# Optimization experiments

Measured on AMD Instinct MI355X. Metric: run time of the kernel, lower is better.

## Reference

```python
import jax, jax.numpy as jnp
import numpy as np

N_NODES = 100000
N_EDGES = 3200000
N_FEAT = 256
N_FILT = 256


def setup_inputs() -> dict:
    key = jax.random.key(0)
    k1, k2, k3, k4, k5 = jax.random.split(key, 5)
    # Xavier-normal-ish filters: std = sqrt(2/(fan_in+fan_out))
    std = (2.0 / (N_FEAT + N_FILT)) ** 0.5
    filters = jax.random.normal(k1, (N_FEAT, N_FILT), dtype=jnp.float32) * std
    x = jax.random.normal(k2, (N_NODES, N_FEAT), dtype=jnp.float32)
    edge_row = jax.random.randint(k3, (N_EDGES,), 0, N_NODES, dtype=jnp.int32)
    edge_col = jax.random.randint(k4, (N_EDGES,), 0, N_NODES, dtype=jnp.int32)
    edge_weight = jax.random.uniform(k5, (N_EDGES,), dtype=jnp.float32)
    return {"x": x, "filters": filters, "edge_row": edge_row,
            "edge_col": edge_col, "edge_weight": edge_weight}


def reference(x, filters, edge_row, edge_col, edge_weight):
    # XF = x @ filters  -> [N, K]
    XF = jnp.matmul(x, filters)
    # out = transform @ XF, transform given in COO form:
    # out[r] = sum_{e: row[e]==r} weight[e] * XF[col[e]]
    msgs = edge_weight[:, None] * XF[edge_col]          # [E, K] gather
    out = jax.ops.segment_sum(msgs, edge_row, num_segments=N_NODES)  # [N, K] scatter-add
    return out
```

## Files before the change

### kernel.cpp

```cpp
#include <hip/hip_runtime.h>

#define NF 256
#define NK 256
#define NBKT 512
#define TILEA 8192

typedef __attribute__((ext_vector_type(8))) short bf16x8;
typedef __attribute__((ext_vector_type(4))) float f32x4;

__device__ __forceinline__ ushort f2bf(float f) {
  uint u = __float_as_uint(f);
  return (ushort)((u + 0x7fffu + ((u >> 16) & 1u)) >> 16);
}
__device__ __forceinline__ float bf2f(ushort h) {
  return __uint_as_float(((uint)h) << 16);
}

__global__ __launch_bounds__(256) void prelude(const float* __restrict__ F,
                                               ushort* __restrict__ Ft,
                                               const int* __restrict__ erow,
                                               int* __restrict__ bcnt, int nE) {
  __shared__ int h[NBKT];
  if (blockIdx.x < NF) {
    int k = blockIdx.x;
    int n = threadIdx.x;
    Ft[(size_t)n * NF + k] = f2bf(F[(size_t)k * NK + n]);
    return;
  }
  const int bid = blockIdx.x - NF;
  const int nb = gridDim.x - NF;
  h[threadIdx.x] = 0;
  h[threadIdx.x + 256] = 0;
  __syncthreads();
  for (int e = bid * 256 + threadIdx.x; e < nE; e += nb * 256)
    atomicAdd(&h[erow[e] >> 8], 1);
  __syncthreads();
  int v0 = h[threadIdx.x], v1 = h[threadIdx.x + 256];
  if (v0) atomicAdd(&bcnt[threadIdx.x], v0);
  if (v1) atomicAdd(&bcnt[threadIdx.x + 256], v1);
}

__global__ __launch_bounds__(256) void gemm_mfma(const float* __restrict__ x,
                                                 const ushort* __restrict__ Ft,
                                                 ushort* __restrict__ XFh, int M) {
  __shared__ ushort As[32 * NF];
  const int t = threadIdx.x;
  const int row0 = blockIdx.x * 32;

  const float4* xv = (const float4*)(x + (size_t)row0 * NF);
#pragma unroll
  for (int j = 0; j < 8; ++j) {
    int idx = j * 256 + t;
    int r = idx >> 6;
    int c4 = idx & 63;
    float4 v = make_float4(0.f, 0.f, 0.f, 0.f);
    if (row0 + r < M) v = xv[idx];
    ushort4 hh = make_ushort4(f2bf(v.x), f2bf(v.y), f2bf(v.z), f2bf(v.w));
    uint boff = (uint)(r * 512 + c4 * 8);
    boff ^= (uint)((r & 7) << 4);
    *(ushort4*)((char*)As + boff) = hh;
  }
  __syncthreads();

  const int lane = t & 63;
  const int wv = t >> 6;
  const int arow = lane & 15;
  const int kg = lane >> 4;

  bf16x8 afr[2][8];
#pragma unroll
  for (int rt = 0; rt < 2; ++rt) {
#pragma unroll
    for (int kk = 0; kk < 8; ++kk) {
      int r = rt * 16 + arow;
      uint boff = (uint)(r * 512 + kk * 64 + kg * 16);
      boff ^= (uint)((r & 7) << 4);
      afr[rt][kk] = *(const bf16x8*)((const char*)As + boff);
    }
  }

  f32x4 acc[2][4];
#pragma unroll
  for (int rt = 0; rt < 2; ++rt)
#pragma unroll
    for (int f = 0; f < 4; ++f) acc[rt][f] = (f32x4){0.f, 0.f, 0.f, 0.f};

  const int ncol0 = wv * 64;
#pragma unroll
  for (int f = 0; f < 4; ++f) {
    const ushort* bp = Ft + (size_t)(ncol0 + f * 16 + arow) * NF + kg * 8;
#pragma unroll
    for (int kk = 0; kk < 8; ++kk) {
      bf16x8 bfr = *(const bf16x8*)(bp + kk * 32);
      acc[0][f] = __builtin_amdgcn_mfma_f32_16x16x32_bf16(afr[0][kk], bfr, acc[0][f], 0, 0, 0);
      acc[1][f] = __builtin_amdgcn_mfma_f32_16x16x32_bf16(afr[1][kk], bfr, acc[1][f], 0, 0, 0);
    }
  }

#pragma unroll
  for (int rt = 0; rt < 2; ++rt) {
#pragma unroll
    for (int f = 0; f < 4; ++f) {
      int col = ncol0 + f * 16 + arow;
#pragma unroll
      for (int rg = 0; rg < 4; ++rg) {
        int row = row0 + rt * 16 + kg * 4 + rg;
        if (row < M) XFh[(size_t)row * NK + col] = f2bf(acc[rt][f][rg]);
      }
    }
  }
}

__global__ __launch_bounds__(512) void scan_bbase(const int* __restrict__ bcnt,
                                                  int* __restrict__ bbase,
                                                  int* __restrict__ bcursor) {
  __shared__ int s[NBKT];
  int t = threadIdx.x;
  int v = bcnt[t];
  s[t] = v;
  __syncthreads();
  for (int d = 1; d < NBKT; d <<= 1) {
    int tmp = (t >= d) ? s[t - d] : 0;
    __syncthreads();
    s[t] += tmp;
    __syncthreads();
  }
  int excl = s[t] - v;
  bbase[t] = excl;
  bcursor[t * 16] = excl;
}

__global__ __launch_bounds__(512) void bin_coarse(const int* __restrict__ erow,
                                                  const int* __restrict__ ecol,
                                                  const float* __restrict__ ew,
                                                  int* __restrict__ bcursor,
                                                  int2* __restrict__ tmpCW, int nE) {
  __shared__ int h[NBKT];
  __shared__ int lb[NBKT];
  __shared__ int gb[NBKT];
  __shared__ int2 pay[TILEA];
  const int t = threadIdx.x;
  const int base = blockIdx.x * TILEA;

  h[t] = 0;
  __syncthreads();

  int rnk[16], bb[16], loc[16];
#pragma unroll
  for (int k = 0; k < 16; ++k) {
    int i = base + k * 512 + t;
    rnk[k] = -1; bb[k] = 0; loc[k] = 0;
    if (i < nE) {
      int row = erow[i];
      bb[k] = row >> 8;
      loc[k] = row & 255;
      rnk[k] = atomicAdd(&h[bb[k]], 1);
    }
  }
  __syncthreads();

  int hv = h[t];
  lb[t] = hv;
  __syncthreads();
  for (int d = 1; d < NBKT; d <<= 1) {
    int tmp = (t >= d) ? lb[t - d] : 0;
    __syncthreads();
    lb[t] += tmp;
    __syncthreads();
  }
  int ex = lb[t] - hv;
  __syncthreads();
  lb[t] = ex;
  if (hv > 0) gb[t] = atomicAdd(&bcursor[t * 16], hv);
  __syncthreads();

#pragma unroll
  for (int k = 0; k < 16; ++k) {
    int i = base + k * 512 + t;
    if (i < nE) {
      int pos = lb[bb[k]] + rnk[k];
      pay[pos] = make_int2(ecol[i] | (loc[k] << 20), __float_as_int(ew[i]));
    }
  }
  __syncthreads();

  const int wv = t >> 6, lane = t & 63;
  for (int b = wv; b < NBKT; b += 8) {
    int len = h[b];
    if (!len) continue;
    int lbase = lb[b], gbase = gb[b];
    for (int off = lane; off < len; off += 64)
      tmpCW[gbase + off] = pay[lbase + off];
  }
}

__global__ __launch_bounds__(256) void bin_fine(const int2* __restrict__ tmpCW,
                                                const int* __restrict__ bbase,
                                                const int* __restrict__ bcnt,
                                                int* __restrict__ offsets,
                                                int2* __restrict__ cw,
                                                int nNodes, int nE) {
  __shared__ int hist[256];
  __shared__ int cur[256];
  const int b = blockIdx.x;
  const int t = threadIdx.x;
  const int base = bbase[b];
  const int n = bcnt[b];

  hist[t] = 0;
  __syncthreads();
  for (int i = t; i < n; i += 256)
    atomicAdd(&hist[((uint)tmpCW[base + i].x) >> 20], 1);
  __syncthreads();

  int hv = hist[t];
  cur[t] = hv;
  __syncthreads();
  for (int d = 1; d < 256; d <<= 1) {
    int tmp = (t >= d) ? cur[t - d] : 0;
    __syncthreads();
    cur[t] += tmp;
    __syncthreads();
  }
  int ex = cur[t] - hv;
  __syncthreads();
  cur[t] = ex;
  int node = (b << 8) + t;
  if (node < nNodes) offsets[node] = base + ex;
  if (b == 0 && t == 0) offsets[nNodes] = nE;
  __syncthreads();

  for (int i = t; i < n; i += 256) {
    int2 v = tmpCW[base + i];
    int local = ((uint)v.x) >> 20;
    int d = base + atomicAdd(&cur[local], 1);
    cw[d] = make_int2(v.x & 0xFFFFF, v.y);
  }
}

__global__ __launch_bounds__(256) void gather_bf16(const ushort* __restrict__ XFh,
                                                   const int* __restrict__ offsets,
                                                   const int2* __restrict__ cw,
                                                   f32x4* __restrict__ outv,
                                                   int nNodes) {
  const int lane = threadIdx.x & 63;
  const int node = (blockIdx.x * blockDim.x + threadIdx.x) >> 6;
  if (node >= nNodes) return;
  const int start = offsets[node];
  const int end = offsets[node + 1];
  const ushort4* XV = (const ushort4*)XFh;

  float ax = 0.f, ay = 0.f, az = 0.f, aw = 0.f;
  for (int base = start; base < end; base += 64) {
    int n = end - base;
    if (n > 64) n = 64;
    int2 e = make_int2(0, 0);
    if (lane < n) {
      long long raw = __builtin_nontemporal_load((const long long*)(cw + base + lane));
      e.x = (int)(raw & 0xFFFFFFFFll);
      e.y = (int)(raw >> 32);
    }
    int skey = (lane < n) ? ((e.x << 6) | lane) : ((0xFFFFF << 6) | lane);
    int sval = e.y;
#pragma unroll
    for (int k = 2; k <= 64; k <<= 1) {
#pragma unroll
      for (int j = k >> 1; j > 0; j >>= 1) {
        int pk = __shfl_xor(skey, j);
        int pv = __shfl_xor(sval, j);
        bool take_min = ((lane & k) == 0) == ((lane & j) == 0);
        bool keep = (take_min == (skey < pk));
        skey = keep ? skey : pk;
        sval = keep ? sval : pv;
      }
    }
    e.x = ((uint)skey) >> 6;
    e.y = sval;

    int j = 0;
    for (; j + 7 < n; j += 8) {
      int c0 = __shfl(e.x, j),     c1 = __shfl(e.x, j + 1);
      int c2 = __shfl(e.x, j + 2), c3 = __shfl(e.x, j + 3);
      int c4 = __shfl(e.x, j + 4), c5 = __shfl(e.x, j + 5);
      int c6 = __shfl(e.x, j + 6), c7 = __shfl(e.x, j + 7);
      float w0 = __int_as_float(__shfl(e.y, j));
      float w1 = __int_as_float(__shfl(e.y, j + 1));
      float w2 = __int_as_float(__shfl(e.y, j + 2));
      float w3 = __int_as_float(__shfl(e.y, j + 3));
      float w4 = __int_as_float(__shfl(e.y, j + 4));
      float w5 = __int_as_float(__shfl(e.y, j + 5));
      float w6 = __int_as_float(__shfl(e.y, j + 6));
      float w7 = __int_as_float(__shfl(e.y, j + 7));
      ushort4 v0 = XV[(size_t)c0 * 64 + lane];
      ushort4 v1 = XV[(size_t)c1 * 64 + lane];
      ushort4 v2 = XV[(size_t)c2 * 64 + lane];
      ushort4 v3 = XV[(size_t)c3 * 64 + lane];
      ushort4 v4 = XV[(size_t)c4 * 64 + lane];
      ushort4 v5 = XV[(size_t)c5 * 64 + lane];
      ushort4 v6 = XV[(size_t)c6 * 64 + lane];
      ushort4 v7 = XV[(size_t)c7 * 64 + lane];
      ax += w0 * bf2f(v0.x); ay += w0 * bf2f(v0.y); az += w0 * bf2f(v0.z); aw += w0 * bf2f(v0.w);
      ax += w1 * bf2f(v1.x); ay += w1 * bf2f(v1.y); az += w1 * bf2f(v1.z); aw += w1 * bf2f(v1.w);
      ax += w2 * bf2f(v2.x); ay += w2 * bf2f(v2.y); az += w2 * bf2f(v2.z); aw += w2 * bf2f(v2.w);
      ax += w3 * bf2f(v3.x); ay += w3 * bf2f(v3.y); az += w3 * bf2f(v3.z); aw += w3 * bf2f(v3.w);
      ax += w4 * bf2f(v4.x); ay += w4 * bf2f(v4.y); az += w4 * bf2f(v4.z); aw += w4 * bf2f(v4.w);
      ax += w5 * bf2f(v5.x); ay += w5 * bf2f(v5.y); az += w5 * bf2f(v5.z); aw += w5 * bf2f(v5.w);
      ax += w6 * bf2f(v6.x); ay += w6 * bf2f(v6.y); az += w6 * bf2f(v6.z); aw += w6 * bf2f(v6.w);
      ax += w7 * bf2f(v7.x); ay += w7 * bf2f(v7.y); az += w7 * bf2f(v7.z); aw += w7 * bf2f(v7.w);
    }
    for (; j + 3 < n; j += 4) {
      int c0 = __shfl(e.x, j),     c1 = __shfl(e.x, j + 1);
      int c2 = __shfl(e.x, j + 2), c3 = __shfl(e.x, j + 3);
      float w0 = __int_as_float(__shfl(e.y, j));
      float w1 = __int_as_float(__shfl(e.y, j + 1));
      float w2 = __int_as_float(__shfl(e.y, j + 2));
      float w3 = __int_as_float(__shfl(e.y, j + 3));
      ushort4 v0 = XV[(size_t)c0 * 64 + lane];
      ushort4 v1 = XV[(size_t)c1 * 64 + lane];
      ushort4 v2 = XV[(size_t)c2 * 64 + lane];
      ushort4 v3 = XV[(size_t)c3 * 64 + lane];
      ax += w0 * bf2f(v0.x); ay += w0 * bf2f(v0.y); az += w0 * bf2f(v0.z); aw += w0 * bf2f(v0.w);
      ax += w1 * bf2f(v1.x); ay += w1 * bf2f(v1.y); az += w1 * bf2f(v1.z); aw += w1 * bf2f(v1.w);
      ax += w2 * bf2f(v2.x); ay += w2 * bf2f(v2.y); az += w2 * bf2f(v2.z); aw += w2 * bf2f(v2.w);
      ax += w3 * bf2f(v3.x); ay += w3 * bf2f(v3.y); az += w3 * bf2f(v3.z); aw += w3 * bf2f(v3.w);
    }
    for (; j < n; ++j) {
      int c0 = __shfl(e.x, j);
      float w0 = __int_as_float(__shfl(e.y, j));
      ushort4 v0 = XV[(size_t)c0 * 64 + lane];
      ax += w0 * bf2f(v0.x); ay += w0 * bf2f(v0.y); az += w0 * bf2f(v0.z); aw += w0 * bf2f(v0.w);
    }
  }
  f32x4 r; r.x = ax; r.y = ay; r.z = az; r.w = aw;
  __builtin_nontemporal_store(r, &outv[(size_t)node * 64 + lane]);
}

__global__ __launch_bounds__(256) void gemm_xf(const float* __restrict__ x,
                                               const float* __restrict__ F,
                                               float* __restrict__ XF, int M) {
  __shared__ float xs[64][NF];
  const int t = threadIdx.x;
  const int row0 = blockIdx.x * 64;
  const int rows = min(64, M - row0);
  const float4* xv = (const float4*)(x + (size_t)row0 * NF);
  float4* xsv = (float4*)&xs[0][0];
#pragma unroll
  for (int j = 0; j < 16; ++j) {
    int i = j * 256 + t;
    int r = i >> 6;
    float4 v;
    if (r < rows) v = xv[i];
    else          v = make_float4(0.f, 0.f, 0.f, 0.f);
    xsv[i] = v;
  }
  __syncthreads();
  const int r0 = (t >> 5) * 8;
  const int c0 = blockIdx.y * 128 + (t & 31) * 4;
  float acc[8][4];
#pragma unroll
  for (int r = 0; r < 8; ++r)
#pragma unroll
    for (int c = 0; c < 4; ++c) acc[r][c] = 0.f;
  for (int k = 0; k < NF; k += 4) {
    float4 f0 = *(const float4*)(F + (size_t)(k + 0) * NK + c0);
    float4 f1 = *(const float4*)(F + (size_t)(k + 1) * NK + c0);
    float4 f2 = *(const float4*)(F + (size_t)(k + 2) * NK + c0);
    float4 f3 = *(const float4*)(F + (size_t)(k + 3) * NK + c0);
#pragma unroll
    for (int r = 0; r < 8; ++r) {
      float4 xr = *(const float4*)&xs[r0 + r][k];
      acc[r][0] += xr.x * f0.x + xr.y * f1.x + xr.z * f2.x + xr.w * f3.x;
      acc[r][1] += xr.x * f0.y + xr.y * f1.y + xr.z * f2.y + xr.w * f3.y;
      acc[r][2] += xr.x * f0.z + xr.y * f1.z + xr.z * f2.z + xr.w * f3.z;
      acc[r][3] += xr.x * f0.w + xr.y * f1.w + xr.z * f2.w + xr.w * f3.w;
    }
  }
#pragma unroll
  for (int r = 0; r < 8; ++r) {
    int row = r0 + r;
    if (row < rows) {
      float4 v = make_float4(acc[r][0], acc[r][1], acc[r][2], acc[r][3]);
      *(float4*)(XF + (size_t)(row0 + row) * NK + c0) = v;
    }
  }
}

__global__ __launch_bounds__(256) void scatter_edges(
    const float* __restrict__ XF, const int* __restrict__ erow,
    const int* __restrict__ ecol, const float* __restrict__ ew,
    float* __restrict__ out, int nE) {
  const int lane = threadIdx.x & 63;
  const int wid = (blockIdx.x * blockDim.x + threadIdx.x) >> 6;
  const int nwaves = (gridDim.x * blockDim.x) >> 6;
  for (int e = wid; e < nE; e += nwaves) {
    const int r = erow[e];
    const int c = ecol[e];
    const float w = ew[e];
    float4 v = *(const float4*)(XF + (size_t)c * NK + lane * 4);
    float* dst = out + (size_t)r * NK + lane * 4;
    atomicAdd(dst + 0, w * v.x);
    atomicAdd(dst + 1, w * v.y);
    atomicAdd(dst + 2, w * v.z);
    atomicAdd(dst + 3, w * v.w);
  }
}

static inline size_t align16(size_t x) { return (x + 15) & ~(size_t)15; }

extern "C" void kernel_launch(void* const* d_in, const int* in_sizes, int n_in,
                              void* d_out, int out_size, void* d_ws, size_t ws_size,
                              hipStream_t stream) {
  const float* x  = (const float*)d_in[0];
  const float* F  = (const float*)d_in[1];
  const int* erow = (const int*)d_in[2];
  const int* ecol = (const int*)d_in[3];
  const float* ew = (const float*)d_in[4];
  float* out      = (float*)d_out;

  const int M      = in_sizes[0] / NF;
  const int nE     = in_sizes[2];
  const int nNodes = out_size / NK;

  char* base = (char*)d_ws;
  size_t off = 0;
  ushort* XFh  = (ushort*)(base + off); off += align16((size_t)M * NK * sizeof(ushort));
  ushort* Ft   = (ushort*)(base + off); off += align16((size_t)NF * NK * sizeof(ushort));
  int* offsets = (int*)(base + off);    off += align16(((size_t)nNodes + 1) * sizeof(int));
  int* bcnt    = (int*)(base + off);    off += align16(NBKT * sizeof(int));
  int* bbase   = (int*)(base + off);    off += align16(NBKT * sizeof(int));
  int* bcursor = (int*)(base + off);    off += align16((size_t)NBKT * 16 * sizeof(int));
  int2* tmpCW  = (int2*)(base + off);   off += align16((size_t)nE * sizeof(int2));
  int2* cw     = (int2*)(base + off);   off += align16((size_t)nE * sizeof(int2));
  const size_t needed = off;

  const int nb2 = (nNodes + 255) >> 8;
  const bool ok = (ws_size >= needed) && (nb2 <= NBKT) &&
                  (nNodes < (1 << 20)) && (M < (1 << 20));

  if (ok) {
    hipMemsetAsync(bcnt, 0, NBKT * sizeof(int), stream);
    prelude<<<NF + 2048, 256, 0, stream>>>(F, Ft, erow, bcnt, nE);
    gemm_mfma<<<(M + 31) / 32, 256, 0, stream>>>(x, Ft, XFh, M);
    scan_bbase<<<1, NBKT, 0, stream>>>(bcnt, bbase, bcursor);
    bin_coarse<<<(nE + TILEA - 1) / TILEA, 512, 0, stream>>>(erow, ecol, ew,
                                                             bcursor, tmpCW, nE);
    bin_fine<<<nb2, 256, 0, stream>>>(tmpCW, bbase, bcnt, offsets, cw, nNodes, nE);
    int gblocks = (nNodes + 3) / 4;
    gather_bf16<<<gblocks, 256, 0, stream>>>(XFh, offsets, cw, (f32x4*)out, nNodes);
  } else {
    float* XF = (float*)d_ws;
    dim3 gg((M + 63) / 64, NK / 128);
    gemm_xf<<<gg, 256, 0, stream>>>(x, F, XF, M);
    hipMemsetAsync(d_out, 0, (size_t)out_size * sizeof(float), stream);
    scatter_edges<<<2048, 256, 0, stream>>>(XF, erow, ecol, ew, out, nE);
  }
}
```

Baseline: 427.6 us.

## Split gather into two feature-half passes for cache locality

Replaces the single gather kernel with two launches, each handling 128 of the 256 output features with 2-wide bf16 loads per lane. The goal is to halve the working set of the gathered XF table per pass so that random row accesses hit in cache more often. In exchange, edge lists are read and bitonic-sorted twice, and each lane's loads shrink, which raises instruction and memory request overhead per byte.

```diff
diff --git a/kernel.cpp b/kernel.cpp
--- a/kernel.cpp
+++ b/kernel.cpp
@@ -7,6 +7,7 @@
 
 typedef __attribute__((ext_vector_type(8))) short bf16x8;
 typedef __attribute__((ext_vector_type(4))) float f32x4;
+typedef __attribute__((ext_vector_type(2))) float f32x2;
 
 __device__ __forceinline__ ushort f2bf(float f) {
   uint u = __float_as_uint(f);
@@ -238,19 +239,20 @@
   }
 }
 
-__global__ __launch_bounds__(256) void gather_bf16(const ushort* __restrict__ XFh,
+__global__ __launch_bounds__(256) void gather_half(const ushort* __restrict__ XFh,
                                                    const int* __restrict__ offsets,
                                                    const int2* __restrict__ cw,
-                                                   f32x4* __restrict__ outv,
-                                                   int nNodes) {
+                                                   f32x2* __restrict__ outv,
+                                                   int nNodes, int half) {
   const int lane = threadIdx.x & 63;
   const int node = (blockIdx.x * blockDim.x + threadIdx.x) >> 6;
   if (node >= nNodes) return;
   const int start = offsets[node];
   const int end = offsets[node + 1];
-  const ushort4* XV = (const ushort4*)XFh;
-
-  float ax = 0.f, ay = 0.f, az = 0.f, aw = 0.f;
+  const ushort2* XV = (const ushort2*)XFh;
+  const int fo = half * 64 + lane;
+
+  float ax = 0.f, ay = 0.f;
   for (int base = start; base < end; base += 64) {
     int n = end - base;
     if (n > 64) n = 64;
@@ -291,22 +293,22 @@
       float w5 = __int_as_float(__shfl(e.y, j + 5));
       float w6 = __int_as_float(__shfl(e.y, j + 6));
       float w7 = __int_as_float(__shfl(e.y, j + 7));
-      ushort4 v0 = XV[(size_t)c0 * 64 + lane];
-      ushort4 v1 = XV[(size_t)c1 * 64 + lane];
-      ushort4 v2 = XV[(size_t)c2 * 64 + lane];
-      ushort4 v3 = XV[(size_t)c3 * 64 + lane];
-      ushort4 v4 = XV[(size_t)c4 * 64 + lane];
-      ushort4 v5 = XV[(size_t)c5 * 64 + lane];
-      ushort4 v6 = XV[(size_t)c6 * 64 + lane];
-      ushort4 v7 = XV[(size_t)c7 * 64 + lane];
-      ax += w0 * bf2f(v0.x); ay += w0 * bf2f(v0.y); az += w0 * bf2f(v0.z); aw += w0 * bf2f(v0.w);
-      ax += w1 * bf2f(v1.x); ay += w1 * bf2f(v1.y); az += w1 * bf2f(v1.z); aw += w1 * bf2f(v1.w);
-      ax += w2 * bf2f(v2.x); ay += w2 * bf2f(v2.y); az += w2 * bf2f(v2.z); aw += w2 * bf2f(v2.w);
-      ax += w3 * bf2f(v3.x); ay += w3 * bf2f(v3.y); az += w3 * bf2f(v3.z); aw += w3 * bf2f(v3.w);
-      ax += w4 * bf2f(v4.x); ay += w4 * bf2f(v4.y); az += w4 * bf2f(v4.z); aw += w4 * bf2f(v4.w);
-      ax += w5 * bf2f(v5.x); ay += w5 * bf2f(v5.y); az += w5 * bf2f(v5.z); aw += w5 * bf2f(v5.w);
-      ax += w6 * bf2f(v6.x); ay += w6 * bf2f(v6.y); az += w6 * bf2f(v6.z); aw += w6 * bf2f(v6.w);
-      ax += w7 * bf2f(v7.x); ay += w7 * bf2f(v7.y); az += w7 * bf2f(v7.z); aw += w7 * bf2f(v7.w);
+      ushort2 v0 = XV[(size_t)c0 * 128 + fo];
+      ushort2 v1 = XV[(size_t)c1 * 128 + fo];
+      ushort2 v2 = XV[(size_t)c2 * 128 + fo];
+      ushort2 v3 = XV[(size_t)c3 * 128 + fo];
+      ushort2 v4 = XV[(size_t)c4 * 128 + fo];
+      ushort2 v5 = XV[(size_t)c5 * 128 + fo];
+      ushort2 v6 = XV[(size_t)c6 * 128 + fo];
+      ushort2 v7 = XV[(size_t)c7 * 128 + fo];
+      ax += w0 * bf2f(v0.x); ay += w0 * bf2f(v0.y);
+      ax += w1 * bf2f(v1.x); ay += w1 * bf2f(v1.y);
+      ax += w2 * bf2f(v2.x); ay += w2 * bf2f(v2.y);
+      ax += w3 * bf2f(v3.x); ay += w3 * bf2f(v3.y);
+      ax += w4 * bf2f(v4.x); ay += w4 * bf2f(v4.y);
+      ax += w5 * bf2f(v5.x); ay += w5 * bf2f(v5.y);
+      ax += w6 * bf2f(v6.x); ay += w6 * bf2f(v6.y);
+      ax += w7 * bf2f(v7.x); ay += w7 * bf2f(v7.y);
     }
     for (; j + 3 < n; j += 4) {
       int c0 = __shfl(e.x, j),     c1 = __shfl(e.x, j + 1);
@@ -315,24 +317,24 @@
       float w1 = __int_as_float(__shfl(e.y, j + 1));
       float w2 = __int_as_float(__shfl(e.y, j + 2));
       float w3 = __int_as_float(__shfl(e.y, j + 3));
-      ushort4 v0 = XV[(size_t)c0 * 64 + lane];
-      ushort4 v1 = XV[(size_t)c1 * 64 + lane];
-      ushort4 v2 = XV[(size_t)c2 * 64 + lane];
-      ushort4 v3 = XV[(size_t)c3 * 64 + lane];
-      ax += w0 * bf2f(v0.x); ay += w0 * bf2f(v0.y); az += w0 * bf2f(v0.z); aw += w0 * bf2f(v0.w);
-      ax += w1 * bf2f(v1.x); ay += w1 * bf2f(v1.y); az += w1 * bf2f(v1.z); aw += w1 * bf2f(v1.w);
-      ax += w2 * bf2f(v2.x); ay += w2 * bf2f(v2.y); az += w2 * bf2f(v2.z); aw += w2 * bf2f(v2.w);
-      ax += w3 * bf2f(v3.x); ay += w3 * bf2f(v3.y); az += w3 * bf2f(v3.z); aw += w3 * bf2f(v3.w);
+      ushort2 v0 = XV[(size_t)c0 * 128 + fo];
+      ushort2 v1 = XV[(size_t)c1 * 128 + fo];
+      ushort2 v2 = XV[(size_t)c2 * 128 + fo];
+      ushort2 v3 = XV[(size_t)c3 * 128 + fo];
+      ax += w0 * bf2f(v0.x); ay += w0 * bf2f(v0.y);
+      ax += w1 * bf2f(v1.x); ay += w1 * bf2f(v1.y);
+      ax += w2 * bf2f(v2.x); ay += w2 * bf2f(v2.y);
+      ax += w3 * bf2f(v3.x); ay += w3 * bf2f(v3.y);
     }
     for (; j < n; ++j) {
       int c0 = __shfl(e.x, j);
       float w0 = __int_as_float(__shfl(e.y, j));
-      ushort4 v0 = XV[(size_t)c0 * 64 + lane];
-      ax += w0 * bf2f(v0.x); ay += w0 * bf2f(v0.y); az += w0 * bf2f(v0.z); aw += w0 * bf2f(v0.w);
-    }
-  }
-  f32x4 r; r.x = ax; r.y = ay; r.z = az; r.w = aw;
-  __builtin_nontemporal_store(r, &outv[(size_t)node * 64 + lane]);
+      ushort2 v0 = XV[(size_t)c0 * 128 + fo];
+      ax += w0 * bf2f(v0.x); ay += w0 * bf2f(v0.y);
+    }
+  }
+  f32x2 r; r.x = ax; r.y = ay;
+  __builtin_nontemporal_store(r, &outv[(size_t)node * 128 + fo]);
 }
 
 __global__ __launch_bounds__(256) void gemm_xf(const float* __restrict__ x,
@@ -446,7 +448,8 @@
                                                              bcursor, tmpCW, nE);
     bin_fine<<<nb2, 256, 0, stream>>>(tmpCW, bbase, bcnt, offsets, cw, nNodes, nE);
     int gblocks = (nNodes + 3) / 4;
-    gather_bf16<<<gblocks, 256, 0, stream>>>(XFh, offsets, cw, (f32x4*)out, nNodes);
+    gather_half<<<gblocks, 256, 0, stream>>>(XFh, offsets, cw, (f32x2*)out, nNodes, 0);
+    gather_half<<<gblocks, 256, 0, stream>>>(XFh, offsets, cw, (f32x2*)out, nNodes, 1);
   } else {
     float* XF = (float*)d_ws;
     dim3 gg((M + 63) / 64, NK / 128);
```

New measurement: 434.6 us. About the same (+1.6%).
